# Kernel optimization log

Hardware: AMD Instinct MI355X
Metric: run time of the kernel (lower is better)

The kernel has to match this reference:

```python
import jax, jax.numpy as jnp
import numpy as np

BUFFER_SIZE = 1024
N_BANDS = 2049
N_SPEC = 4
FRAME_SIZE = 2 * (N_BANDS - 1)  # 4096
EPS = 1e-10


def _hann_periodic(n):
    k = np.arange(n, dtype=np.float64)
    return (0.5 * (1.0 - np.cos(2.0 * np.pi * k / n))).astype(np.float32)


def _build_windows():
    # Mirrors _build_windows with nonlinearity=0 (single filterbank).
    base = _hann_periodic(FRAME_SIZE) / (FRAME_SIZE / 4.0)
    win_scale = float(base.sum())
    wins = [base.copy()]
    for lvl in range(1, N_SPEC):
        stride = 1 << lvl
        small = base[::stride][: FRAME_SIZE // stride]
        w = np.zeros(FRAME_SIZE, dtype=np.float32)
        w[-(FRAME_SIZE // stride):] = small
        w *= win_scale / w.sum()
        wins.append(w)
    return [jnp.asarray(w) for w in wins]


WINDOWS = _build_windows()


def _forward(x):
    # x: (B, BUFFER_SIZE). Fresh (reset) state: time buffers are zeros,
    # spectrogram/left-boundary buffers are +1e6 (identity for min).
    B = x.shape[0]
    T = 1 << (N_SPEC - 1)  # finest time grid = output columns
    out = jnp.full((B, N_BANDS, T), 1.0e6, dtype=x.dtype)
    pad = jnp.zeros((B, FRAME_SIZE), dtype=x.dtype)
    concat = jnp.concatenate([pad, x], axis=-1)  # (B, FRAME_SIZE + BUFFER_SIZE)
    for lvl in range(N_SPEC):
        chunk = BUFFER_SIZE >> lvl
        nfr = 1 << lvl  # sub-frames at this level
        # Overlap-save sliding windows: frame i starts at offset chunk + i*chunk
        frames = jnp.stack(
            [concat[:, chunk + i * chunk: chunk + i * chunk + FRAME_SIZE] for i in range(nfr)],
            axis=1,
        )  # (B, nfr, FRAME_SIZE)
        spec = jnp.fft.rfft(frames * WINDOWS[lvl][None, None, :], n=FRAME_SIZE, axis=-1)
        power = jnp.transpose(spec.real ** 2 + spec.imag ** 2, (0, 2, 1))  # (B, N_BANDS, nfr)
        # Upsample coarse-time levels to the finest grid (tile replication, the
        # streaming moving-max/min buffers realize this in the original) and
        # take the min across scales (buffers initialised to 1e6 = +inf for min).
        out = jnp.minimum(out, jnp.repeat(power, T // nfr, axis=-1))
    return 10.0 * jnp.log10(jnp.maximum(out, EPS))  # power -> dB


def setup_inputs() -> dict:
    key = jax.random.key(0)
    x = jax.random.normal(key, (1024, BUFFER_SIZE), dtype=jnp.float32)
    return {"x": x}


def reference(x):
    return _forward(x)
```

## Files before the change

kernel.cpp:

```cpp
#include <hip/hip_runtime.h>
#include <hip/hip_fp16.h>
#include <math.h>

#define NBANDS 2049
#define NF 4096
#define NC 2048
#define BUF 1024
#define THREADS 512
#define R2C 0.70710678118654752f

__device__ __forceinline__ int SW(int i) { return i ^ (i >> 2) ^ (i >> 6); }

__device__ __forceinline__ int posrev10(int j) {
  return ((j & 3) << 9) | (((j >> 2) & 3) << 7) | (((j >> 4) & 3) << 5) |
         (((j >> 6) & 3) << 3) | (((j >> 8) & 3) << 1);
}

struct Smem {
  alignas(16) float xs[BUF];
  alignas(16) float zreA[NC];
  alignas(16) float zimA[NC];
  alignas(16) float zreB[NC];
  alignas(16) float zimB[NC];
  alignas(16) float zreC[NC];
  alignas(16) float zimC[NC];
};

struct State {
  float2 W[5];
  float2 Ub;
  float2 U1;
  float so;
  float s1a[5], s1b[5];
  float s2a[5], s2b[5];
  __half2 oh[4][5];
};

__device__ __forceinline__ float2 cmul(float2 a, float2 b) {
  return make_float2(a.x * b.x - a.y * b.y, a.x * b.y + a.y * b.x);
}

template <int L>
__device__ __forceinline__ float cheb(float c) {
  #pragma unroll
  for (int i = 0; i < L; ++i) c = 2.0f * c * c - 1.0f;
  return c;
}

template <int L>
__device__ __forceinline__ void fused_s1(float* __restrict__ re, float* __restrict__ im,
                                         const Smem& sm, const State& st, int off) {
  const int n = threadIdx.x;
  constexpr int M = NF >> L;
  constexpr float ws = (float)(1 << L) * (0.5f / 1024.0f);
  const int lo = 512 - (min(off, M) >> 1);
  float dr = 0.0f, di = 0.0f;
  if (n >= lo) {
    const int idx = 2 * n + off - 1024;
    const float2 xv = *(const float2*)&sm.xs[idx];
    const float cE = cheb<L>(-st.W[0].y);
    const float cO = cheb<L>(st.so);
    dr = ws * (1.0f - cE) * xv.x;
    di = ws * (1.0f - cO) * xv.y;
  }
  const float2 W = st.W[0];
  const float2 W2 = make_float2(W.x * W.x - W.y * W.y, 2.0f * W.x * W.y);
  const float2 W3 = cmul(W, W2);
  const int p0 = SW(n), p1 = SW(n + 512), p2 = SW(n + 1024), p3 = SW(n + 1536);
  re[p0] = dr;                       im[p0] = di;
  re[p1] = -di * W.x - dr * W.y;     im[p1] = -di * W.y + dr * W.x;
  re[p2] = -(dr * W2.x - di * W2.y); im[p2] = -(dr * W2.y + di * W2.x);
  re[p3] =  di * W3.x + dr * W3.y;   im[p3] =  di * W3.y - dr * W3.x;
}

__device__ __forceinline__ void bfly4(float* __restrict__ re, float* __restrict__ im,
                                      int i0, int i1, int i2, int i3,
                                      float2 W, float2 W2, float2 W3) {
  float ar = re[i0], ai = im[i0];
  float br = re[i1], bi = im[i1];
  float cr = re[i2], ci = im[i2];
  float dr = re[i3], di = im[i3];
  float t0r = ar + cr, t0i = ai + ci;
  float t1r = ar - cr, t1i = ai - ci;
  float t2r = br + dr, t2i = bi + di;
  float t3r = br - dr, t3i = bi - di;
  re[i0] = t0r + t2r; im[i0] = t0i + t2i;
  float y1r = t1r + t3i, y1i = t1i - t3r;
  re[i1] = y1r * W.x - y1i * W.y;  im[i1] = y1r * W.y + y1i * W.x;
  float y2r = t0r - t2r, y2i = t0i - t2i;
  re[i2] = y2r * W2.x - y2i * W2.y; im[i2] = y2r * W2.y + y2i * W2.x;
  float y3r = t1r - t3i, y3i = t1i + t3r;
  re[i3] = y3r * W3.x - y3i * W3.y; im[i3] = y3r * W3.y + y3i * W3.x;
}

template <int LM, int NFR>
__device__ __forceinline__ void radix4p(Smem& sm, float2 W) {
  const int j = threadIdx.x;
  const int m = 1 << LM;
  const int base = ((j >> LM) << (LM + 2)) | (j & (m - 1));
  const int i0 = SW(base), i1 = SW(base + m), i2 = SW(base + 2 * m), i3 = SW(base + 3 * m);
  float2 W2 = make_float2(W.x * W.x - W.y * W.y, 2.0f * W.x * W.y);
  float2 W3 = cmul(W, W2);
  bfly4(sm.zreA, sm.zimA, i0, i1, i2, i3, W, W2, W3);
  if constexpr (NFR >= 2) bfly4(sm.zreB, sm.zimB, i0, i1, i2, i3, W, W2, W3);
  if constexpr (NFR >= 3) bfly4(sm.zreC, sm.zimC, i0, i1, i2, i3, W, W2, W3);
}

__device__ __forceinline__ void pair_powers(const float* __restrict__ re,
                                            const float* __restrict__ im,
                                            int kp, float2 U, float& pp, float& pm) {
  const int k1 = kp & (NC - 1);
  const int k2 = (NC - kp) & (NC - 1);
  const int q1 = SW(posrev10(k1 & 1023));
  const int q2 = SW(posrev10(k2 & 1023));
  const float s1 = (k1 & 1024) ? -1.0f : 1.0f;
  const float s2 = (k2 & 1024) ? -1.0f : 1.0f;
  const float2 vr1 = *(const float2*)&re[q1 & ~1];
  const float2 vi1 = *(const float2*)&im[q1 & ~1];
  const float2 vr2 = *(const float2*)&re[q2 & ~1];
  const float2 vi2 = *(const float2*)&im[q2 & ~1];
  const bool o1 = (q1 & 1), o2 = (q2 & 1);
  const float zkr = o1 ? (vr1.y + s1 * vr1.x) : (vr1.x + s1 * vr1.y);
  const float zki = o1 ? (vi1.y + s1 * vi1.x) : (vi1.x + s1 * vi1.y);
  const float zmr = o2 ? (vr2.y + s2 * vr2.x) : (vr2.x + s2 * vr2.y);
  const float zmi = o2 ? (vi2.y + s2 * vi2.x) : (vi2.x + s2 * vi2.y);
  const float Ex = 0.5f * (zkr + zmr), Ey = 0.5f * (zki - zmi);
  const float Ox = 0.5f * (zki + zmi), Oy = -0.5f * (zkr - zmr);
  const float Vx = U.x * Ox - U.y * Oy, Vy = U.x * Oy + U.y * Ox;
  const float ax = Ex + Vx, ay = Ey + Vy;
  const float bx = Ex - Vx, by = Ey - Vy;
  pp = ax * ax + ay * ay;
  pm = bx * bx + by * by;
}

template <int ACT, int COL, int SLOT>
__device__ __forceinline__ void act(State& st, float p) {
  if constexpr (ACT == 0)      st.s1a[SLOT] = fminf(p, 1.0e6f);
  else if constexpr (ACT == 1) st.s1b[SLOT] = fminf(p, 1.0e6f);
  else if constexpr (ACT == 2) { st.s1a[SLOT] = fminf(st.s1a[SLOT], p); st.s1b[SLOT] = fminf(st.s1b[SLOT], p); }
  else if constexpr (ACT == 3) st.s2a[SLOT] = fminf(st.s1a[SLOT], p);
  else if constexpr (ACT == 4) st.s2b[SLOT] = fminf(st.s1a[SLOT], p);
  else if constexpr (ACT == 5) st.s2a[SLOT] = fminf(st.s1b[SLOT], p);
  else if constexpr (ACT == 6) st.s2b[SLOT] = fminf(st.s1b[SLOT], p);
  else {
    const float base = (ACT == 7) ? st.s2a[SLOT] : st.s2b[SLOT];
    const float db = 10.0f * log10f(fmaxf(fminf(base, p), 1.0e-10f));
    if constexpr (COL & 1) st.oh[COL >> 1][SLOT].y = __float2half_rn(db);
    else                   st.oh[COL >> 1][SLOT].x = __float2half_rn(db);
  }
}

template <int ACT, int COL>
__device__ __forceinline__ void unpack_frame(const float* __restrict__ re,
                                             const float* __restrict__ im,
                                             State& st) {
  const int t = threadIdx.x;
  float pp, pm;
  pair_powers(re, im, t, st.Ub, pp, pm);
  act<ACT, COL, 0>(st, pp);
  act<ACT, COL, 1>(st, pm);
  pair_powers(re, im, 512 + t, st.U1, pp, pm);
  act<ACT, COL, 2>(st, pp);
  act<ACT, COL, 3>(st, pm);
  if (t == 0) {
    const float zr = re[0] - re[1];
    const float zi = im[0] - im[1];
    act<ACT, COL, 4>(st, zr * zr + zi * zi);
  }
}

template <int LA, int AA, int CA, int LB, int AB, int CB, int LC, int AC, int CC, int NFR>
__device__ __forceinline__ void pass(Smem& sm, State& st, int offA, int offB, int offC) {
  __syncthreads();
  fused_s1<LA>(sm.zreA, sm.zimA, sm, st, offA);
  if constexpr (NFR >= 2) fused_s1<LB>(sm.zreB, sm.zimB, sm, st, offB);
  if constexpr (NFR >= 3) fused_s1<LC>(sm.zreC, sm.zimC, sm, st, offC);
  __syncthreads(); radix4p<7, NFR>(sm, st.W[1]);
  __syncthreads(); radix4p<5, NFR>(sm, st.W[2]);
  __syncthreads(); radix4p<3, NFR>(sm, st.W[3]);
  __syncthreads(); radix4p<1, NFR>(sm, st.W[4]);
  __syncthreads();
  unpack_frame<AA, CA>(sm.zreA, sm.zimA, st);
  if constexpr (NFR >= 2) unpack_frame<AB, CB>(sm.zreB, sm.zimB, st);
  if constexpr (NFR >= 3) unpack_frame<AC, CC>(sm.zreC, sm.zimC, st);
}

__device__ __forceinline__ void store_all(const State& st, float* __restrict__ outb) {
  const int t = threadIdx.x;
  #pragma unroll
  for (int sl = 0; sl < 5; ++sl) {
    if (sl < 4 || t == 0) {
      const int band = (sl == 0) ? t : (sl == 1) ? 2048 - t
                     : (sl == 2) ? 512 + t : (sl == 3) ? 1536 - t : 1024;
      float* bp = outb + (size_t)band * 8;
      *(float4*)(bp)     = make_float4(__half2float(st.oh[0][sl].x), __half2float(st.oh[0][sl].y),
                                       __half2float(st.oh[1][sl].x), __half2float(st.oh[1][sl].y));
      *(float4*)(bp + 4) = make_float4(__half2float(st.oh[2][sl].x), __half2float(st.oh[2][sl].y),
                                       __half2float(st.oh[3][sl].x), __half2float(st.oh[3][sl].y));
    }
  }
}

__global__ __launch_bounds__(THREADS, 2) void spec_kernel(const float* __restrict__ x,
                                                          float* __restrict__ out) {
  __shared__ Smem sm;
  State st;
  const int tid = threadIdx.x;
  const int b = blockIdx.x;
  const float* xb = x + (size_t)b * BUF;
  #pragma unroll
  for (int i = tid; i < BUF; i += THREADS) sm.xs[i] = xb[i];
  {
    float sn, cs;
    sincospif((float)tid * (1.0f / 1024.0f), &sn, &cs);         st.W[0] = make_float2(cs, -sn);
    sincospif((float)(tid & 127) * (1.0f / 256.0f), &sn, &cs);  st.W[1] = make_float2(cs, -sn);
    sincospif((float)(tid & 31) * (1.0f / 64.0f), &sn, &cs);    st.W[2] = make_float2(cs, -sn);
    sincospif((float)(tid & 7) * (1.0f / 16.0f), &sn, &cs);     st.W[3] = make_float2(cs, -sn);
    st.W[4] = (tid & 1) ? make_float2(R2C, -R2C) : make_float2(1.0f, 0.0f);
    sincospif((float)tid * (1.0f / 2048.0f), &sn, &cs);         st.Ub = make_float2(cs, -sn);
    st.U1 = cmul(st.Ub, make_float2(R2C, -R2C));
    sincospif((float)(2 * tid + 1) * (1.0f / 2048.0f), &sn, &cs); st.so = sn;
  }
  float* outb = out + (size_t)b * (NBANDS * 8);

  pass<1, 0, 0,  1, 1, 0,  0, 2, 0, 3>(sm, st, 512, 1024, 1024);
  pass<2, 3, 0,  2, 4, 0,  3, 7, 0, 3>(sm, st, 256, 512, 128);
  pass<3, 7, 1,  3, 8, 2,  3, 8, 3, 3>(sm, st, 256, 384, 512);
  pass<2, 5, 0,  2, 6, 0,  3, 7, 4, 3>(sm, st, 768, 1024, 640);
  pass<3, 7, 5,  3, 8, 6,  3, 8, 7, 3>(sm, st, 768, 896, 1024);
  store_all(st, outb);
}

extern "C" void kernel_launch(void* const* d_in, const int* in_sizes, int n_in,
                              void* d_out, int out_size, void* d_ws, size_t ws_size,
                              hipStream_t stream) {
  const float* x = (const float*)d_in[0];
  float* out = (float*)d_out;
  const int B = in_sizes[0] / BUF;
  hipLaunchKernelGGL(spec_kernel, dim3(B), dim3(THREADS), 0, stream, x, out);
}
```

Measured before the change: 96.90 us.

## Replace four radix-4 shared-memory stages with two register radix-16 passes, four frames per pass

The 1024-point FFT's four radix-4 stages, each with its own barrier, become two radix-16 stages held in registers. Each 128-thread group handles one frame, so four frames run per pass and the pass count drops from five to four. The shared-memory swizzle becomes a simpler XOR pattern, which lets the unpack step read aligned float2 pairs without a parity select. This removes barriers and shared-memory round trips at the cost of more registers per thread (32 floats of FFT data) and a larger shared buffer with four frame slots, which may lower occupancy.

```diff
diff --git a/kernel.cpp b/kernel.cpp
--- a/kernel.cpp
+++ b/kernel.cpp
@@ -8,8 +8,12 @@
 #define BUF 1024
 #define THREADS 512
 #define R2C 0.70710678118654752f
-
-__device__ __forceinline__ int SW(int i) { return i ^ (i >> 2) ^ (i >> 6); }
+#define C8  0.92387953251128674f
+#define S8  0.38268343236508978f
+#define C16 0.98078528040323044f
+#define S16 0.19509032201612827f
+
+__device__ __forceinline__ int SWc(int i) { return i ^ (((i >> 5) & 15) << 1); }
 
 __device__ __forceinline__ int posrev10(int j) {
   return ((j & 3) << 9) | (((j >> 2) & 3) << 7) | (((j >> 4) & 3) << 5) |
@@ -18,16 +22,13 @@
 
 struct Smem {
   alignas(16) float xs[BUF];
-  alignas(16) float zreA[NC];
-  alignas(16) float zimA[NC];
-  alignas(16) float zreB[NC];
-  alignas(16) float zimB[NC];
-  alignas(16) float zreC[NC];
-  alignas(16) float zimC[NC];
+  alignas(16) float zre[4][NC];
+  alignas(16) float zim[4][NC];
 };
 
 struct State {
-  float2 W[5];
+  float2 W0;
+  float2 V;
   float2 Ub;
   float2 U1;
   float so;
@@ -58,52 +59,117 @@
   if (n >= lo) {
     const int idx = 2 * n + off - 1024;
     const float2 xv = *(const float2*)&sm.xs[idx];
-    const float cE = cheb<L>(-st.W[0].y);
+    const float cE = cheb<L>(-st.W0.y);
     const float cO = cheb<L>(st.so);
     dr = ws * (1.0f - cE) * xv.x;
     di = ws * (1.0f - cO) * xv.y;
   }
-  const float2 W = st.W[0];
+  const float2 W = st.W0;
   const float2 W2 = make_float2(W.x * W.x - W.y * W.y, 2.0f * W.x * W.y);
   const float2 W3 = cmul(W, W2);
-  const int p0 = SW(n), p1 = SW(n + 512), p2 = SW(n + 1024), p3 = SW(n + 1536);
+  const int X1 = ((n >> 5) & 15) << 1;
+  const int p0 = n ^ X1, p1 = (n + 512) ^ X1, p2 = (n + 1024) ^ X1, p3 = (n + 1536) ^ X1;
   re[p0] = dr;                       im[p0] = di;
   re[p1] = -di * W.x - dr * W.y;     im[p1] = -di * W.y + dr * W.x;
   re[p2] = -(dr * W2.x - di * W2.y); im[p2] = -(dr * W2.y + di * W2.x);
   re[p3] =  di * W3.x + dr * W3.y;   im[p3] =  di * W3.y - dr * W3.x;
 }
 
-__device__ __forceinline__ void bfly4(float* __restrict__ re, float* __restrict__ im,
-                                      int i0, int i1, int i2, int i3,
-                                      float2 W, float2 W2, float2 W3) {
-  float ar = re[i0], ai = im[i0];
-  float br = re[i1], bi = im[i1];
-  float cr = re[i2], ci = im[i2];
-  float dr = re[i3], di = im[i3];
-  float t0r = ar + cr, t0i = ai + ci;
-  float t1r = ar - cr, t1i = ai - ci;
-  float t2r = br + dr, t2i = bi + di;
-  float t3r = br - dr, t3i = bi - di;
-  re[i0] = t0r + t2r; im[i0] = t0i + t2i;
-  float y1r = t1r + t3i, y1i = t1i - t3r;
-  re[i1] = y1r * W.x - y1i * W.y;  im[i1] = y1r * W.y + y1i * W.x;
-  float y2r = t0r - t2r, y2i = t0i - t2i;
-  re[i2] = y2r * W2.x - y2i * W2.y; im[i2] = y2r * W2.y + y2i * W2.x;
-  float y3r = t1r - t3i, y3i = t1i + t3r;
-  re[i3] = y3r * W3.x - y3i * W3.y; im[i3] = y3r * W3.y + y3i * W3.x;
-}
-
-template <int LM, int NFR>
-__device__ __forceinline__ void radix4p(Smem& sm, float2 W) {
-  const int j = threadIdx.x;
-  const int m = 1 << LM;
-  const int base = ((j >> LM) << (LM + 2)) | (j & (m - 1));
-  const int i0 = SW(base), i1 = SW(base + m), i2 = SW(base + 2 * m), i3 = SW(base + 3 * m);
-  float2 W2 = make_float2(W.x * W.x - W.y * W.y, 2.0f * W.x * W.y);
-  float2 W3 = cmul(W, W2);
-  bfly4(sm.zreA, sm.zimA, i0, i1, i2, i3, W, W2, W3);
-  if constexpr (NFR >= 2) bfly4(sm.zreB, sm.zimB, i0, i1, i2, i3, W, W2, W3);
-  if constexpr (NFR >= 3) bfly4(sm.zreC, sm.zimC, i0, i1, i2, i3, W, W2, W3);
+__device__ __forceinline__ void bflyr(float* __restrict__ xr, float* __restrict__ xi,
+                                      int a, int b, int c, int d,
+                                      float Wr, float Wi, float W2r, float W2i,
+                                      float W3r, float W3i) {
+  const float t0r = xr[a] + xr[c], t0i = xi[a] + xi[c];
+  const float t1r = xr[a] - xr[c], t1i = xi[a] - xi[c];
+  const float t2r = xr[b] + xr[d], t2i = xi[b] + xi[d];
+  const float t3r = xr[b] - xr[d], t3i = xi[b] - xi[d];
+  xr[a] = t0r + t2r; xi[a] = t0i + t2i;
+  const float y1r = t1r + t3i, y1i = t1i - t3r;
+  xr[b] = y1r * Wr - y1i * Wi;  xi[b] = y1r * Wi + y1i * Wr;
+  const float y2r = t0r - t2r, y2i = t0i - t2i;
+  xr[c] = y2r * W2r - y2i * W2i; xi[c] = y2r * W2i + y2i * W2r;
+  const float y3r = t1r - t3i, y3i = t1i + t3r;
+  xr[d] = y3r * W3r - y3i * W3i; xi[d] = y3r * W3i + y3i * W3r;
+}
+
+template <int NFR>
+__device__ __forceinline__ void r16a(Smem& sm, const State& st) {
+  const int f = threadIdx.x >> 7;
+  if (f >= NFR) return;
+  const int lt = threadIdx.x & 127;
+  const int c = lt >> 5, r = lt & 31;
+  const int base = c * 512 + r;
+  float* __restrict__ re = sm.zre[f];
+  float* __restrict__ im = sm.zim[f];
+  float xr[16], xi[16];
+  #pragma unroll
+  for (int u = 0; u < 16; ++u) {
+    const int p = (base + 32 * u) ^ (2 * u);
+    xr[u] = re[p]; xi[u] = im[p];
+  }
+  const float ECs[4] = {1.0f, C8, R2C, S8};
+  const float ESs[4] = {0.0f, -S8, -R2C, -C8};
+  #pragma unroll
+  for (int s = 0; s < 4; ++s) {
+    const float Wr = st.V.x * ECs[s] - st.V.y * ESs[s];
+    const float Wi = st.V.x * ESs[s] + st.V.y * ECs[s];
+    const float W2r = Wr * Wr - Wi * Wi, W2i = 2.0f * Wr * Wi;
+    const float W3r = Wr * W2r - Wi * W2i, W3i = Wr * W2i + Wi * W2r;
+    bflyr(xr, xi, s, s + 4, s + 8, s + 12, Wr, Wi, W2r, W2i, W3r, W3i);
+  }
+  const float sqr = st.V.x * st.V.x - st.V.y * st.V.y, sqi = 2.0f * st.V.x * st.V.y;
+  const float Tr = sqr * sqr - sqi * sqi, Ti = 2.0f * sqr * sqi;
+  const float T2r = Tr * Tr - Ti * Ti, T2i = 2.0f * Tr * Ti;
+  const float T3r = Tr * T2r - Ti * T2i, T3i = Tr * T2i + Ti * T2r;
+  #pragma unroll
+  for (int b = 0; b < 4; ++b)
+    bflyr(xr, xi, 4 * b, 4 * b + 1, 4 * b + 2, 4 * b + 3, Tr, Ti, T2r, T2i, T3r, T3i);
+  #pragma unroll
+  for (int u = 0; u < 16; ++u) {
+    const int p = (base + 32 * u) ^ (2 * u);
+    re[p] = xr[u]; im[p] = xi[u];
+  }
+}
+
+template <int NFR>
+__device__ __forceinline__ void r16b(Smem& sm) {
+  const int f = threadIdx.x >> 7;
+  if (f >= NFR) return;
+  const int lt = threadIdx.x & 127;
+  const int c2 = lt >> 1, r2 = lt & 1;
+  const int base = c2 * 32 + r2;
+  const int X = (c2 & 15) << 1;
+  float* __restrict__ re = sm.zre[f];
+  float* __restrict__ im = sm.zim[f];
+  float xr[16], xi[16];
+  #pragma unroll
+  for (int u = 0; u < 16; ++u) {
+    const int p = (base + 2 * u) ^ X;
+    xr[u] = re[p]; xi[u] = im[p];
+  }
+  const float v2r = r2 ? C16 : 1.0f;
+  const float v2i = r2 ? -S16 : 0.0f;
+  const float ECs[4] = {1.0f, C8, R2C, S8};
+  const float ESs[4] = {0.0f, -S8, -R2C, -C8};
+  #pragma unroll
+  for (int s = 0; s < 4; ++s) {
+    const float Wr = v2r * ECs[s] - v2i * ESs[s];
+    const float Wi = v2r * ESs[s] + v2i * ECs[s];
+    const float W2r = Wr * Wr - Wi * Wi, W2i = 2.0f * Wr * Wi;
+    const float W3r = Wr * W2r - Wi * W2i, W3i = Wr * W2i + Wi * W2r;
+    bflyr(xr, xi, s, s + 4, s + 8, s + 12, Wr, Wi, W2r, W2i, W3r, W3i);
+  }
+  const float Tr = r2 ? R2C : 1.0f, Ti = r2 ? -R2C : 0.0f;
+  const float T2r = r2 ? 0.0f : 1.0f, T2i = r2 ? -1.0f : 0.0f;
+  const float T3r = r2 ? -R2C : 1.0f, T3i = r2 ? -R2C : 0.0f;
+  #pragma unroll
+  for (int b = 0; b < 4; ++b)
+    bflyr(xr, xi, 4 * b, 4 * b + 1, 4 * b + 2, 4 * b + 3, Tr, Ti, T2r, T2i, T3r, T3i);
+  #pragma unroll
+  for (int u = 0; u < 16; ++u) {
+    const int p = (base + 2 * u) ^ X;
+    re[p] = xr[u]; im[p] = xi[u];
+  }
 }
 
 __device__ __forceinline__ void pair_powers(const float* __restrict__ re,
@@ -111,19 +177,18 @@
                                             int kp, float2 U, float& pp, float& pm) {
   const int k1 = kp & (NC - 1);
   const int k2 = (NC - kp) & (NC - 1);
-  const int q1 = SW(posrev10(k1 & 1023));
-  const int q2 = SW(posrev10(k2 & 1023));
+  const int q1 = SWc(posrev10(k1 & 1023));
+  const int q2 = SWc(posrev10(k2 & 1023));
   const float s1 = (k1 & 1024) ? -1.0f : 1.0f;
   const float s2 = (k2 & 1024) ? -1.0f : 1.0f;
-  const float2 vr1 = *(const float2*)&re[q1 & ~1];
-  const float2 vi1 = *(const float2*)&im[q1 & ~1];
-  const float2 vr2 = *(const float2*)&re[q2 & ~1];
-  const float2 vi2 = *(const float2*)&im[q2 & ~1];
-  const bool o1 = (q1 & 1), o2 = (q2 & 1);
-  const float zkr = o1 ? (vr1.y + s1 * vr1.x) : (vr1.x + s1 * vr1.y);
-  const float zki = o1 ? (vi1.y + s1 * vi1.x) : (vi1.x + s1 * vi1.y);
-  const float zmr = o2 ? (vr2.y + s2 * vr2.x) : (vr2.x + s2 * vr2.y);
-  const float zmi = o2 ? (vi2.y + s2 * vi2.x) : (vi2.x + s2 * vi2.y);
+  const float2 vr1 = *(const float2*)&re[q1];
+  const float2 vi1 = *(const float2*)&im[q1];
+  const float2 vr2 = *(const float2*)&re[q2];
+  const float2 vi2 = *(const float2*)&im[q2];
+  const float zkr = vr1.x + s1 * vr1.y;
+  const float zki = vi1.x + s1 * vi1.y;
+  const float zmr = vr2.x + s2 * vr2.y;
+  const float zmi = vi2.x + s2 * vi2.y;
   const float Ex = 0.5f * (zkr + zmr), Ey = 0.5f * (zki - zmi);
   const float Ox = 0.5f * (zki + zmi), Oy = -0.5f * (zkr - zmr);
   const float Vx = U.x * Ox - U.y * Oy, Vy = U.x * Oy + U.y * Ox;
@@ -169,20 +234,24 @@
   }
 }
 
-template <int LA, int AA, int CA, int LB, int AB, int CB, int LC, int AC, int CC, int NFR>
-__device__ __forceinline__ void pass(Smem& sm, State& st, int offA, int offB, int offC) {
+template <int LA, int AA, int CA, int LB, int AB, int CB,
+          int LC, int AC, int CC, int LD, int AD, int CD, int NFR>
+__device__ __forceinline__ void pass(Smem& sm, State& st,
+                                     int offA, int offB, int offC, int offD) {
   __syncthreads();
-  fused_s1<LA>(sm.zreA, sm.zimA, sm, st, offA);
-  if constexpr (NFR >= 2) fused_s1<LB>(sm.zreB, sm.zimB, sm, st, offB);
-  if constexpr (NFR >= 3) fused_s1<LC>(sm.zreC, sm.zimC, sm, st, offC);
-  __syncthreads(); radix4p<7, NFR>(sm, st.W[1]);
-  __syncthreads(); radix4p<5, NFR>(sm, st.W[2]);
-  __syncthreads(); radix4p<3, NFR>(sm, st.W[3]);
-  __syncthreads(); radix4p<1, NFR>(sm, st.W[4]);
+  fused_s1<LA>(sm.zre[0], sm.zim[0], sm, st, offA);
+  if constexpr (NFR >= 2) fused_s1<LB>(sm.zre[1], sm.zim[1], sm, st, offB);
+  if constexpr (NFR >= 3) fused_s1<LC>(sm.zre[2], sm.zim[2], sm, st, offC);
+  if constexpr (NFR >= 4) fused_s1<LD>(sm.zre[3], sm.zim[3], sm, st, offD);
   __syncthreads();
-  unpack_frame<AA, CA>(sm.zreA, sm.zimA, st);
-  if constexpr (NFR >= 2) unpack_frame<AB, CB>(sm.zreB, sm.zimB, st);
-  if constexpr (NFR >= 3) unpack_frame<AC, CC>(sm.zreC, sm.zimC, st);
+  r16a<NFR>(sm, st);
+  __syncthreads();
+  r16b<NFR>(sm);
+  __syncthreads();
+  unpack_frame<AA, CA>(sm.zre[0], sm.zim[0], st);
+  if constexpr (NFR >= 2) unpack_frame<AB, CB>(sm.zre[1], sm.zim[1], st);
+  if constexpr (NFR >= 3) unpack_frame<AC, CC>(sm.zre[2], sm.zim[2], st);
+  if constexpr (NFR >= 4) unpack_frame<AD, CD>(sm.zre[3], sm.zim[3], st);
 }
 
 __device__ __forceinline__ void store_all(const State& st, float* __restrict__ outb) {
@@ -212,22 +281,18 @@
   for (int i = tid; i < BUF; i += THREADS) sm.xs[i] = xb[i];
   {
     float sn, cs;
-    sincospif((float)tid * (1.0f / 1024.0f), &sn, &cs);         st.W[0] = make_float2(cs, -sn);
-    sincospif((float)(tid & 127) * (1.0f / 256.0f), &sn, &cs);  st.W[1] = make_float2(cs, -sn);
-    sincospif((float)(tid & 31) * (1.0f / 64.0f), &sn, &cs);    st.W[2] = make_float2(cs, -sn);
-    sincospif((float)(tid & 7) * (1.0f / 16.0f), &sn, &cs);     st.W[3] = make_float2(cs, -sn);
-    st.W[4] = (tid & 1) ? make_float2(R2C, -R2C) : make_float2(1.0f, 0.0f);
-    sincospif((float)tid * (1.0f / 2048.0f), &sn, &cs);         st.Ub = make_float2(cs, -sn);
+    sincospif((float)tid * (1.0f / 1024.0f), &sn, &cs);           st.W0 = make_float2(cs, -sn);
+    sincospif((float)(tid & 31) * (1.0f / 256.0f), &sn, &cs);     st.V  = make_float2(cs, -sn);
+    sincospif((float)tid * (1.0f / 2048.0f), &sn, &cs);           st.Ub = make_float2(cs, -sn);
     st.U1 = cmul(st.Ub, make_float2(R2C, -R2C));
     sincospif((float)(2 * tid + 1) * (1.0f / 2048.0f), &sn, &cs); st.so = sn;
   }
   float* outb = out + (size_t)b * (NBANDS * 8);
 
-  pass<1, 0, 0,  1, 1, 0,  0, 2, 0, 3>(sm, st, 512, 1024, 1024);
-  pass<2, 3, 0,  2, 4, 0,  3, 7, 0, 3>(sm, st, 256, 512, 128);
-  pass<3, 7, 1,  3, 8, 2,  3, 8, 3, 3>(sm, st, 256, 384, 512);
-  pass<2, 5, 0,  2, 6, 0,  3, 7, 4, 3>(sm, st, 768, 1024, 640);
-  pass<3, 7, 5,  3, 8, 6,  3, 8, 7, 3>(sm, st, 768, 896, 1024);
+  pass<1, 0, 0,  1, 1, 0,  0, 2, 0,  2, 3, 0, 4>(sm, st, 512, 1024, 1024, 256);
+  pass<2, 4, 0,  3, 7, 0,  3, 7, 1,  2, 5, 0, 4>(sm, st, 512, 128, 256, 768);
+  pass<3, 8, 2,  3, 8, 3,  2, 6, 0,  3, 7, 4, 4>(sm, st, 384, 512, 1024, 640);
+  pass<3, 7, 5,  3, 8, 6,  3, 8, 7,  0, 0, 0, 3>(sm, st, 768, 896, 1024, 0);
   store_all(st, outb);
 }
 
```

Result: no change. 97.51 us (+0.6%).
